# Performance work log

Hardware: AMD Instinct MI355X
Metric: run time of the kernel (lower is better)

## Reference

```python
import jax, jax.numpy as jnp
import numpy as np

C_CURV = 0.1            # curvature k
SC = float(np.sqrt(C_CURV))
EPS = 1e-7


def _mobius_add(x, y, c):
    x2 = jnp.sum(x * x, -1, keepdims=True)
    y2 = jnp.sum(y * y, -1, keepdims=True)
    xy = jnp.sum(x * y, -1, keepdims=True)
    num = (1 + 2 * c * xy + c * y2) * x + (1 - c * x2) * y
    den = 1 + 2 * c * xy + c * c * x2 * y2
    return num / jnp.maximum(den, 1e-12)


def _mobius_scalarmul(r, x, c):
    sc = jnp.sqrt(c)
    n = jnp.linalg.norm(x, axis=-1, keepdims=True)
    t = jnp.clip(sc * n, EPS, 1.0 - 1e-6)
    return jnp.tanh(r * jnp.arctanh(t)) * x / jnp.maximum(sc * n, EPS)


def setup_inputs() -> dict:
    key = jax.random.key(0)
    k0, k1, k2, k3, k4 = jax.random.split(key, 5)
    B, N, V, D, NC = 64, 1024, 50257, 128, 10
    token_ids = jax.random.randint(k0, (B, N), 0, V)
    mask = jax.random.randint(k1, (B, N), 0, 2).astype(bool)
    emb = (jax.random.normal(k2, (V, D), jnp.float32) * 0.02).at[0].set(0.0)  # pad_id=0 row zeroed
    Wo = jax.random.normal(k3, (D, D + 1), jnp.float32) / np.sqrt(D + 1)
    bo = jnp.zeros((D,), jnp.float32)
    Wf = jax.random.normal(k4, (NC, D), jnp.float32) / np.sqrt(D)
    bf = jnp.zeros((NC,), jnp.float32)
    return {"token_ids": token_ids, "mask": mask, "emb": emb, "Wo": Wo, "bo": bo, "Wf": Wf, "bf": bf}


def reference(token_ids, mask, emb, Wo, bo, Wf, bf):
    c, sc = C_CURV, SC
    D = emb.shape[1]
    # embedding lookup (tangent vectors at origin)
    v = emb[token_ids]                                            # (B,N,D)
    # Lorentz expmap0 -> hyperboloid points in D+1
    nv = jnp.maximum(jnp.linalg.norm(v, axis=-1, keepdims=True), EPS)
    x = jnp.concatenate([jnp.cosh(sc * nv) / sc,
                         jnp.sinh(sc * nv) * v / (sc * nv)], -1)  # (B,N,D+1)
    # single-head attention, scores = -<xi,xj>_L (Lorentz inner), masked softmax
    sgn = jnp.concatenate([-jnp.ones((1,)), jnp.ones((D,))]).astype(x.dtype)
    scores = -jnp.einsum('bid,bjd->bij', x * sgn, x) / np.sqrt(D + 1)
    scores = jnp.where(mask[:, None, :], scores, -1e9)
    w = jax.nn.softmax(scores, axis=-1)
    # riemannian value aggregation: Lorentz centroid (weighted sum renormalized to hyperboloid)
    mu = jnp.einsum('bij,bjd->bid', w, x)
    inner = jnp.einsum('bid,d,bid->bi', mu, sgn, mu)
    mu = mu / (sc * jnp.sqrt(jnp.maximum(-inner, EPS))[..., None])
    # output projection (D+1 -> D) then Poincare expmap0 so points lie in the ball
    u = jnp.einsum('bid,od->bio', mu, Wo) + bo                    # (B,N,D)
    nu = jnp.maximum(jnp.linalg.norm(u, axis=-1, keepdims=True), EPS)
    y = jnp.tanh(sc * nu) * u / (sc * nu)                         # (B,N,D) in ball
    # sequential masked Mobius pooling: left-fold mobius_add over valid tokens, then scalarmul 1/n
    def step(acc, xm):
        xi, mi = xm                                               # (B,D), (B,)
        new = _mobius_add(acc, xi, c)
        return jnp.where(mi[:, None], new, acc), None
    acc0 = jnp.zeros_like(y[:, 0, :])
    acc, _ = jax.lax.scan(step, acc0, (jnp.swapaxes(y, 0, 1), jnp.swapaxes(mask, 0, 1)))
    cnt = jnp.sum(mask, axis=1)
    r = (1.0 / jnp.maximum(cnt, 1))[:, None].astype(y.dtype)
    pooled = _mobius_scalarmul(r, acc, c)
    pooled = jnp.where((cnt > 0)[:, None], pooled, y[:, 0, :])    # empty rows fall back to first token
    # LorentzMLR head: logmap0 then linear
    npn = jnp.maximum(jnp.linalg.norm(pooled, axis=-1, keepdims=True), EPS)
    t = jnp.clip(sc * npn, EPS, 1.0 - 1e-6)
    vlog = jnp.arctanh(t) * pooled / (sc * npn)
    return vlog @ Wf.T + bf                                       # (B, num_classes)
```

## Files before the change

### kernel.cpp

```cpp
#include <hip/hip_runtime.h>
#include <math.h>

#define B_    64
#define N_    1024
#define D_    128
#define DP1   129
#define NC_   10
#define QB    128
#define KT    32
#define SCf   0.31622776601683794f
#define SCALE 0.08804509063256238f

typedef __bf16 bf16x8 __attribute__((ext_vector_type(8)));
typedef float  f32x16 __attribute__((ext_vector_type(16)));
typedef unsigned long long ull;

#define MFMA(a, b, c) __builtin_amdgcn_mfma_f32_32x32x16_bf16((a), (b), (c), 0, 0, 0)

static __device__ __forceinline__ float dpp_add_step(float f, int ctrl, int rmask) {
    if (ctrl == 0x111) { int t = __builtin_amdgcn_update_dpp(0, __builtin_bit_cast(int, f), 0x111, 0xf, 0xf, true); return f + __builtin_bit_cast(float, t); }
    if (ctrl == 0x112) { int t = __builtin_amdgcn_update_dpp(0, __builtin_bit_cast(int, f), 0x112, 0xf, 0xf, true); return f + __builtin_bit_cast(float, t); }
    if (ctrl == 0x114) { int t = __builtin_amdgcn_update_dpp(0, __builtin_bit_cast(int, f), 0x114, 0xf, 0xf, true); return f + __builtin_bit_cast(float, t); }
    if (ctrl == 0x118) { int t = __builtin_amdgcn_update_dpp(0, __builtin_bit_cast(int, f), 0x118, 0xf, 0xf, true); return f + __builtin_bit_cast(float, t); }
    if (ctrl == 0x142 && rmask == 0xa) { int t = __builtin_amdgcn_update_dpp(0, __builtin_bit_cast(int, f), 0x142, 0xa, 0xf, true); return f + __builtin_bit_cast(float, t); }
    { int t = __builtin_amdgcn_update_dpp(0, __builtin_bit_cast(int, f), 0x143, 0xc, 0xf, true); return f + __builtin_bit_cast(float, t); }
}

static __device__ __forceinline__ float wave_sum64(float f) {
    f = dpp_add_step(f, 0x111, 0xf);
    f = dpp_add_step(f, 0x112, 0xf);
    f = dpp_add_step(f, 0x114, 0xf);
    f = dpp_add_step(f, 0x118, 0xf);
    f = dpp_add_step(f, 0x142, 0xa);
    f = dpp_add_step(f, 0x143, 0xc);
    return __builtin_bit_cast(float, __builtin_amdgcn_readlane(__builtin_bit_cast(int, f), 63));
}

static __device__ __forceinline__ float half_sum32(float f, int half) {
    f = dpp_add_step(f, 0x111, 0xf);
    f = dpp_add_step(f, 0x112, 0xf);
    f = dpp_add_step(f, 0x114, 0xf);
    f = dpp_add_step(f, 0x118, 0xf);
    f = dpp_add_step(f, 0x142, 0xa);
    float s0 = __builtin_bit_cast(float, __builtin_amdgcn_readlane(__builtin_bit_cast(int, f), 31));
    float s1 = __builtin_bit_cast(float, __builtin_amdgcn_readlane(__builtin_bit_cast(int, f), 63));
    return half ? s1 : s0;
}

static __device__ __forceinline__ float readlane_f(float v, int lane) {
    return __builtin_bit_cast(float, __builtin_amdgcn_readlane(__builtin_bit_cast(int, v), lane));
}

static __device__ __forceinline__ bf16x8 ld_lds8(const __bf16* p) {
    union { bf16x8 v; ull q[2]; } u;
    u.q[0] = *(const ull*)(p);
    u.q[1] = *(const ull*)(p + 4);
    return u.v;
}

__global__ __launch_bounds__(256) void k_detect_mask(const int* __restrict__ mask_w,
                                                     int* __restrict__ flag) {
    __shared__ int bad;
    if (threadIdx.x == 0) bad = 0;
    __syncthreads();
    int local = 0;
    for (int i = threadIdx.x; i < 16384; i += 256) {
        int v = mask_w[i];
        if (v != 0 && v != 1) local = 1;
    }
    if (local) atomicOr(&bad, 1);
    __syncthreads();
    if (threadIdx.x == 0) *flag = bad;
}

static __device__ __forceinline__ int read_mask(const int* mw, int is_i8, int idx) {
    if (is_i8) return (int)((const unsigned char*)mw)[idx];
    return mw[idx];
}

__global__ __launch_bounds__(256) void k_prep_wo(const float* __restrict__ Wo,
                                                 __bf16* __restrict__ Woh,
                                                 __bf16* __restrict__ Wol) {
    int idx = blockIdx.x * 256 + threadIdx.x;
    if (idx >= 128 * 144) return;
    int o = idx / 144, d = idx - o * 144;
    float v = (d < DP1) ? Wo[o * DP1 + d] : 0.f;
    __bf16 h = (__bf16)v;
    Woh[idx] = h;
    Wol[idx] = (__bf16)(v - (float)h);
}

__global__ __launch_bounds__(256) void k_prep(const int* __restrict__ tok,
                                              const float* __restrict__ emb,
                                              __bf16* __restrict__ Xh, __bf16* __restrict__ Xl,
                                              float* __restrict__ X0g, float* __restrict__ X128g) {
    __shared__ float Xf[64][132];
    const int t = threadIdx.x, w = t >> 6, l = t & 63;
    const int base = blockIdx.x * 64;
    for (int it = 0; it < 16; ++it) {
        const int tk = w * 16 + it;
        const int id = tok[base + tk];
        const float2 v = ((const float2*)(emb + (size_t)id * D_))[l];
        float s = wave_sum64(v.x * v.x + v.y * v.y);
        float nv = fmaxf(sqrtf(s), 1e-7f);
        float a = SCf * nv;
        float a2 = a * a;
        float shc, ch;
        if (a < 0.5f) {
            shc = 1.f + a2 * (1.f/6.f) * (1.f + a2 * (1.f/20.f) * (1.f + a2 * (1.f/42.f)));
            ch  = 1.f + a2 * 0.5f * (1.f + a2 * (1.f/12.f) * (1.f + a2 * (1.f/30.f)));
        } else {
            float ea = __expf(a), ei = 1.f / ea;
            ch = 0.5f * (ea + ei);
            shc = 0.5f * (ea - ei) / a;
        }
        Xf[tk][1 + 2 * l] = v.x * shc;
        Xf[tk][2 + 2 * l] = v.y * shc;
        if (l == 0) Xf[tk][0] = ch / SCf;
    }
    __syncthreads();
    const int tk2 = t >> 2, dg = (t & 3) * 32;
    for (int i = 0; i < 32; i += 8) {
        bf16x8 hv, lv;
        #pragma unroll
        for (int j = 0; j < 8; ++j) {
            float f = Xf[tk2][dg + i + j];
            __bf16 h = (__bf16)f;
            hv[j] = h;
            lv[j] = (__bf16)(f - (float)h);
        }
        *(bf16x8*)(Xh + (size_t)(base + tk2) * D_ + dg + i) = hv;
        *(bf16x8*)(Xl + (size_t)(base + tk2) * D_ + dg + i) = lv;
    }
    if (t < 64) {
        X0g[base + t]   = Xf[t][0];
        X128g[base + t] = Xf[t][D_];
    }
}

__global__ __launch_bounds__(256, 2) void k_attn(
        const __bf16* __restrict__ Xh, const __bf16* __restrict__ Xl,
        const float* __restrict__ X0g, const float* __restrict__ X128g,
        const int* __restrict__ mask, const int* __restrict__ mflag,
        const __bf16* __restrict__ Woh, const __bf16* __restrict__ Wol,
        const float* __restrict__ bo,
        float* __restrict__ Y, float* __restrict__ Y2) {
    extern __shared__ char smem[];
    __bf16* KB = (__bf16*)smem;
    __bf16* Pb = (__bf16*)(smem + 33792);
    __shared__ float K0s[2][KT];
    __shared__ float K128s[2][KT];
    __shared__ int   Ms[2][KT];

    const int b    = blockIdx.x;
    const int qb   = blockIdx.y * QB;
    const int t    = threadIdx.x;
    const int w    = t >> 6;
    const int l    = t & 63;
    const int l31  = l & 31;
    const int half = l >> 5;
    const int is8  = *mflag;

    const size_t qrow = (size_t)(b * N_ + qb + w * 32 + l31);
    bf16x8 qfh[8], qfl[8];
    #pragma unroll
    for (int ks = 0; ks < 8; ++ks) {
        qfh[ks] = *(const bf16x8*)(Xh + qrow * D_ + ks * 16 + half * 8);
        qfl[ks] = *(const bf16x8*)(Xl + qrow * D_ + ks * 16 + half * 8);
    }
    float q0[16], q128[16];
    #pragma unroll
    for (int r = 0; r < 16; ++r) {
        const int qr = (r & 3) + 8 * (r >> 2) + 4 * half;
        q0[r]   = X0g[b * N_ + qb + w * 32 + qr];
        q128[r] = X128g[b * N_ + qb + w * 32 + qr];
    }

    const int skey = t >> 3, sck = t & 7;
    bf16x8 svh0, svh1, svl0, svl1;
    float  sK0 = 0.f, sK128 = 0.f;
    int    sM = 0;
    auto ldg_tile = [&](int kt) {
        const size_t kr = (size_t)(b * N_ + kt * KT + skey);
        svh0 = *(const bf16x8*)(Xh + kr * D_ + sck * 16);
        svh1 = *(const bf16x8*)(Xh + kr * D_ + sck * 16 + 8);
        svl0 = *(const bf16x8*)(Xl + kr * D_ + sck * 16);
        svl1 = *(const bf16x8*)(Xl + kr * D_ + sck * 16 + 8);
        if (t < KT) {
            sK0   = X0g[b * N_ + kt * KT + t];
            sK128 = X128g[b * N_ + kt * KT + t];
            sM    = read_mask(mask, is8, b * N_ + kt * KT + t);
        }
    };
    auto st_tile = [&](int buf) {
        __bf16* KH = KB + buf * 8448;
        __bf16* KL = KH + 4224;
        union { bf16x8 v; ull q[2]; } u;
        u.v = svh0; *(ull*)(KH + skey * 132 + sck * 16)      = u.q[0]; *(ull*)(KH + skey * 132 + sck * 16 + 4)  = u.q[1];
        u.v = svh1; *(ull*)(KH + skey * 132 + sck * 16 + 8)  = u.q[0]; *(ull*)(KH + skey * 132 + sck * 16 + 12) = u.q[1];
        u.v = svl0; *(ull*)(KL + skey * 132 + sck * 16)      = u.q[0]; *(ull*)(KL + skey * 132 + sck * 16 + 4)  = u.q[1];
        u.v = svl1; *(ull*)(KL + skey * 132 + sck * 16 + 8)  = u.q[0]; *(ull*)(KL + skey * 132 + sck * 16 + 12) = u.q[1];
        if (t < KT) { K0s[buf][t] = sK0; K128s[buf][t] = sK128; Ms[buf][t] = sM; }
    };

    f32x16 accM[4] = {};
    float  mu128p[16] = {};

    ldg_tile(0);
    st_tile(0);

    for (int kt = 0; kt < N_ / KT; ++kt) {
        __syncthreads();
        const int cur = kt & 1;
        const int ktn = (kt < 31) ? kt + 1 : 31;
        ldg_tile(ktn);

        const __bf16* KH = KB + cur * 8448;
        const __bf16* KL = KH + 4224;

        f32x16 accS = {};
        #pragma unroll
        for (int ks = 0; ks < 8; ++ks) {
            bf16x8 bh = ld_lds8(KH + l31 * 132 + ks * 16 + half * 8);
            bf16x8 bl = ld_lds8(KL + l31 * 132 + ks * 16 + half * 8);
            accS = MFMA(qfh[ks], bh, accS);
            accS = MFMA(qfh[ks], bl, accS);
            accS = MFMA(qfl[ks], bh, accS);
        }
        const float k0v = K0s[cur][l31], k128v = K128s[cur][l31];
        const int   mv  = Ms[cur][l31];
        #pragma unroll
        for (int r = 0; r < 16; ++r) {
            float sc = (2.f * q0[r] * k0v - accS[r] - q128[r] * k128v) * SCALE;
            float e  = mv ? __expf(sc) : 0.f;
            mu128p[r] += e * k128v;
            __bf16 eh = (__bf16)e;
            __bf16 el = (__bf16)(e - (float)eh);
            const int qr = (r & 3) + 8 * (r >> 2) + 4 * half;
            Pb[(w * 2 + 0) * 1152 + qr * 36 + l31] = eh;
            Pb[(w * 2 + 1) * 1152 + qr * 36 + l31] = el;
        }

        #pragma unroll
        for (int ks = 0; ks < 2; ++ks) {
            bf16x8 ah = ld_lds8(Pb + (w * 2 + 0) * 1152 + l31 * 36 + ks * 16 + half * 8);
            bf16x8 al = ld_lds8(Pb + (w * 2 + 1) * 1152 + l31 * 36 + ks * 16 + half * 8);
            #pragma unroll
            for (int nt = 0; nt < 4; ++nt) {
                const int cmp = nt * 32 + l31;
                bf16x8 bh, bl;
                #pragma unroll
                for (int j = 0; j < 8; ++j) {
                    const int key = ks * 16 + half * 8 + j;
                    bh[j] = KH[key * 132 + cmp];
                    bl[j] = KL[key * 132 + cmp];
                }
                accM[nt] = MFMA(ah, bh, accM[nt]);
                accM[nt] = MFMA(ah, bl, accM[nt]);
                accM[nt] = MFMA(al, bh, accM[nt]);
            }
        }

        st_tile(cur ^ 1);
    }

    #pragma unroll
    for (int r = 0; r < 16; ++r) mu128p[r] = half_sum32(mu128p[r], half);
    float rno[16];
    #pragma unroll
    for (int r = 0; r < 16; ++r) {
        float p = 0.f;
        #pragma unroll
        for (int nt = 0; nt < 4; ++nt) p += accM[nt][r] * accM[nt][r];
        if (l31 == 0) p -= 2.f * accM[0][r] * accM[0][r];
        p = half_sum32(p, half);
        float negI = -(p + mu128p[r] * mu128p[r]);
        negI = fmaxf(negI, 1e-7f);
        rno[r] = 1.f / (SCf * sqrtf(negI));
    }
    #pragma unroll
    for (int nt = 0; nt < 4; ++nt)
        #pragma unroll
        for (int r = 0; r < 16; ++r) accM[nt][r] *= rno[r];
    #pragma unroll
    for (int r = 0; r < 16; ++r) mu128p[r] *= rno[r];

    __syncthreads();
    __bf16* MuA = (__bf16*)smem + w * (32 * 148);
    #pragma unroll
    for (int r = 0; r < 16; ++r) {
        const int qr = (r & 3) + 8 * (r >> 2) + 4 * half;
        #pragma unroll
        for (int nt = 0; nt < 4; ++nt)
            MuA[qr * 148 + nt * 32 + l31] = (__bf16)accM[nt][r];
        if (l31 == 0) MuA[qr * 148 + 128] = (__bf16)mu128p[r];
        if (l31 >= 1 && l31 <= 15) MuA[qr * 148 + 128 + l31] = (__bf16)0.f;
    }
    bf16x8 Ah[9];
    #pragma unroll
    for (int ks = 0; ks < 9; ++ks) Ah[ks] = ld_lds8(MuA + l31 * 148 + ks * 16 + half * 8);
    #pragma unroll
    for (int r = 0; r < 16; ++r) {
        const int qr = (r & 3) + 8 * (r >> 2) + 4 * half;
        #pragma unroll
        for (int nt = 0; nt < 4; ++nt) {
            float m = accM[nt][r];
            MuA[qr * 148 + nt * 32 + l31] = (__bf16)(m - (float)(__bf16)m);
        }
        if (l31 == 0) {
            float m = mu128p[r];
            MuA[qr * 148 + 128] = (__bf16)(m - (float)(__bf16)m);
        }
    }
    bf16x8 Al[9];
    #pragma unroll
    for (int ks = 0; ks < 9; ++ks) Al[ks] = ld_lds8(MuA + l31 * 148 + ks * 16 + half * 8);

    f32x16 accU[4] = {};
    #pragma unroll
    for (int ks = 0; ks < 9; ++ks) {
        #pragma unroll
        for (int nt = 0; nt < 4; ++nt) {
            bf16x8 bh = *(const bf16x8*)(Woh + (size_t)(nt * 32 + l31) * 144 + ks * 16 + half * 8);
            bf16x8 bl = *(const bf16x8*)(Wol + (size_t)(nt * 32 + l31) * 144 + ks * 16 + half * 8);
            accU[nt] = MFMA(Ah[ks], bh, accU[nt]);
            accU[nt] = MFMA(Ah[ks], bl, accU[nt]);
            accU[nt] = MFMA(Al[ks], bh, accU[nt]);
        }
    }

    float bov[4];
    #pragma unroll
    for (int nt = 0; nt < 4; ++nt) bov[nt] = bo[nt * 32 + l31];
    #pragma unroll
    for (int r = 0; r < 16; ++r) {
        float p = 0.f;
        #pragma unroll
        for (int nt = 0; nt < 4; ++nt) {
            float uv = accU[nt][r] + bov[nt];
            accU[nt][r] = uv;
            p += uv * uv;
        }
        float nn = half_sum32(p, half);
        float nu = fmaxf(sqrtf(nn), 1e-7f);
        float aa = SCf * nu;
        float cf = tanhf(aa) / aa;
        const int qr = (r & 3) + 8 * (r >> 2) + 4 * half;
        const size_t row = (size_t)(b * N_ + qb + w * 32 + qr);
        #pragma unroll
        for (int nt = 0; nt < 4; ++nt)
            Y[row * D_ + nt * 32 + l31] = accU[nt][r] * cf;
        if (l31 == 0) Y2[row] = nn * cf * cf;
    }
}

__global__ __launch_bounds__(256) void k_gram(const float* __restrict__ Y,
                                              float* __restrict__ G) {
    const int c = blockIdx.x, b = blockIdx.y;
    const int t = threadIdx.x, w = t >> 6, l = t & 63;
    const int l31 = l & 31, half = l >> 5;
    const int rt = w >> 1, ct = w & 1;
    const size_t base = (size_t)(b * N_ + c * 64);
    const float* Ar = Y + (base + rt * 32 + l31) * D_;
    const float* Br = Y + (base + ct * 32 + l31) * D_;
    f32x16 acc = {};
    #pragma unroll
    for (int ks = 0; ks < 8; ++ks) {
        const int c0 = ks * 16 + half * 8;
        float4 a0 = *(const float4*)(Ar + c0);
        float4 a1 = *(const float4*)(Ar + c0 + 4);
        float4 b0 = *(const float4*)(Br + c0);
        float4 b1 = *(const float4*)(Br + c0 + 4);
        float av[8] = {a0.x, a0.y, a0.z, a0.w, a1.x, a1.y, a1.z, a1.w};
        float bv[8] = {b0.x, b0.y, b0.z, b0.w, b1.x, b1.y, b1.z, b1.w};
        bf16x8 ah, al, bh, bl;
        #pragma unroll
        for (int j = 0; j < 8; ++j) {
            __bf16 h = (__bf16)av[j]; ah[j] = h; al[j] = (__bf16)(av[j] - (float)h);
            __bf16 g = (__bf16)bv[j]; bh[j] = g; bl[j] = (__bf16)(bv[j] - (float)g);
        }
        acc = MFMA(ah, bh, acc);
        acc = MFMA(ah, bl, acc);
        acc = MFMA(al, bh, acc);
    }
    float* Gb = G + ((size_t)(b * 16 + c) << 12);
    #pragma unroll
    for (int r = 0; r < 16; ++r) {
        const int row = rt * 32 + (r & 3) + 8 * (r >> 2) + 4 * half;
        Gb[row * 64 + ct * 32 + l31] = acc[r];
    }
}

__global__ __launch_bounds__(64, 1) void k_pool(const float* __restrict__ Y,
                                                const float* __restrict__ Y2,
                                                const float* __restrict__ G,
                                                const int* __restrict__ mask,
                                                const int* __restrict__ mflag,
                                                const float* __restrict__ Wf,
                                                const float* __restrict__ bf_,
                                                float* __restrict__ out) {
    __shared__ float  prt[64][65];
    __shared__ double vb[D_];
    const int b = blockIdx.x, l = threadIdx.x;
    const int is8 = *mflag;

    int cl = 0;
    for (int i = l; i < N_; i += 64) cl += read_mask(mask, is8, b * N_ + i);
    const int cntT = (int)(wave_sum64((float)cl) + 0.5f);

    const float2* __restrict__ Yp = (const float2*)(Y + (size_t)b * N_ * D_) + l;
    const float*  __restrict__ Gp = G + ((size_t)b << 16) + l;
    const float*  __restrict__ Pp = Y2 + b * N_;

    float  GA[64], GB[64];
    float  py2A, py2B;
    int    msA, msB;
    float2 yring[2][16];

    #pragma unroll
    for (int i = 0; i < 64; ++i) GA[i] = Gp[i * 64];
    py2A = Pp[l];
    msA  = read_mask(mask, is8, b * N_ + l);
    #pragma unroll
    for (int k = 0; k < 16; ++k) yring[0][k] = Yp[(size_t)k * 64];

    float U0 = 0.f, U1 = 0.f, g = 0.f, Dh = 1.f, P = 0.f;

    auto chunk = [&](int c, float (&Gc)[64], float (&Gn)[64],
                     float py2c, float& py2n, int msc, int& msn) {
        const int cn = (c < 15) ? c + 1 : 15;
        #pragma unroll
        for (int i = 0; i < 64; ++i) Gn[i] = Gp[cn * 4096 + i * 64];
        py2n = Pp[cn * 64 + l];
        msn  = read_mask(mask, is8, b * N_ + cn * 64 + l);

        #pragma unroll
        for (int q = 0; q < 4; ++q) {
            #pragma unroll
            for (int k = 0; k < 16; ++k) {
                int gs = c * 64 + (q + 1) * 16 + k;
                if (gs > N_ - 1) gs = N_ - 1;
                yring[(q + 1) & 1][k] = Yp[(size_t)gs * 64];
            }
            #pragma unroll
            for (int k = 0; k < 16; ++k) {
                const int ir = q * 16 + k;
                const float2 yv  = yring[q & 1][k];
                const float  Gv  = Gc[ir];
                const float  py2 = readlane_f(py2c, ir);
                const bool   m   = (__builtin_amdgcn_readlane(msc, ir) != 0);
                const float Dsq   = Dh * Dh;
                const float Bh    = fmaf(-0.1f, P, Dsq);
                const float Donep = Dh * fmaf(0.1f, py2, 1.f);
                const float tP    = (0.01f * py2) * P;
                const float puy  = readlane_f(g, ir);
                const float Ahat = fmaf(0.2f, puy, Donep);
                float dh = fmaf(Dh, fmaf(0.2f, puy, Dh), tP);
                dh = fmaxf(dh, 1e-12f * Dsq);
                const float Draw = m ? dh : Dh;
                const float Am   = m ? Ahat : 1.f;
                const float Bm   = m ? Bh   : 0.f;
                const float Pn   = fmaf(Am, fmaf(Am, P, (2.f * Bm) * puy), (Bm * Bm) * py2);
                if ((k & 3) == 3) {
                    const int e = ilogbf(Draw);
                    const float Aef = ldexpf(Am, -e);
                    const float Bef = ldexpf(Bm, -e);
                    Dh = ldexpf(Draw, -e);
                    P  = ldexpf(Pn, -2 * e);
                    g  = fmaf(Aef, g, Bef * Gv);
                    U0 = fmaf(Aef, U0, Bef * yv.x);
                    U1 = fmaf(Aef, U1, Bef * yv.y);
                } else {
                    Dh = Draw;
                    P  = Pn;
                    g  = fmaf(Am, g, Bm * Gv);
                    U0 = fmaf(Am, U0, Bm * yv.x);
                    U1 = fmaf(Am, U1, Bm * yv.y);
                }
            }
        }
        if (c < 15) {
            const int nb = (c + 1) * 64;
            #pragma unroll
            for (int k0 = 0; k0 < 64; k0 += 16) {
                float2 tmp[16];
                #pragma unroll
                for (int k = 0; k < 16; ++k) tmp[k] = Yp[(size_t)(nb + k0 + k) * 64];
                #pragma unroll
                for (int k = 0; k < 16; ++k)
                    prt[k0 + k][l] = fmaf(U0, tmp[k].x, U1 * tmp[k].y);
            }
            float s0 = 0.f, s1 = 0.f, s2 = 0.f, s3 = 0.f;
            #pragma unroll
            for (int p = 0; p < 64; p += 4) {
                s0 += prt[l][p];     s1 += prt[l][p + 1];
                s2 += prt[l][p + 2]; s3 += prt[l][p + 3];
            }
            g = (s0 + s1) + (s2 + s3);
        }
    };

    for (int cc = 0; cc < 8; ++cc) {
        chunk(2 * cc,     GA, GB, py2A, py2B, msA, msB);
        chunk(2 * cc + 1, GB, GA, py2B, py2A, msB, msA);
    }

    const double SCd = 0.31622776601683794;
    const double sD = 1.0 / (double)Dh;
    double a0 = sD * (double)U0, a1 = sD * (double)U1;
    double n2 = fmax((double)P * (sD * sD), 0.0);
    double n = sqrt(n2);
    double tt = SCd * n;
    tt = fmin(fmax(tt, 1e-7), 1.0 - 1e-6);
    int cm = cntT > 0 ? cntT : 1;
    float rf = (float)(1.0 / (double)cm);
    double r = (double)rf;
    double dv = fmax(SCd * n, 1e-7);
    double f = tanh(r * atanh(tt)) / dv;
    double p0 = a0 * f, p1 = a1 * f;
    double q2;
    if (cntT == 0) {
        float2 y0v = *(const float2*)(Y + (size_t)(b * N_) * D_ + 2 * l);
        p0 = y0v.x; p1 = y0v.y;
        q2 = (double)Y2[b * N_];
    } else {
        q2 = f * f * n2;
    }
    double npn = fmax(sqrt(q2), 1e-7);
    double t2 = fmin(fmax(SCd * npn, 1e-7), 1.0 - 1e-6);
    double f2 = atanh(t2) / (SCd * npn);
    vb[2 * l]     = p0 * f2;
    vb[2 * l + 1] = p1 * f2;
    __syncthreads();

    if (l < NC_) {
        double o = (double)bf_[l];
        for (int d = 0; d < D_; ++d) o += vb[d] * (double)Wf[l * D_ + d];
        out[b * NC_ + l] = (float)o;
    }
}

extern "C" void kernel_launch(void* const* d_in, const int* in_sizes, int n_in,
                              void* d_out, int out_size, void* d_ws, size_t ws_size,
                              hipStream_t stream) {
    const int*   tok  = (const int*)d_in[0];
    const int*   mask = (const int*)d_in[1];
    const float* emb  = (const float*)d_in[2];
    const float* Wo   = (const float*)d_in[3];
    const float* bo   = (const float*)d_in[4];
    const float* Wf   = (const float*)d_in[5];
    const float* bf_  = (const float*)d_in[6];
    float* out = (float*)d_out;

    char* wsb = (char*)d_ws;
    __bf16* Xh   = (__bf16*)wsb;
    __bf16* Xl   = (__bf16*)(wsb + 16777216);
    float*  X0g  = (float*)(wsb + 33554432);
    float*  X128g= (float*)(wsb + 33816576);
    __bf16* Woh  = (__bf16*)(wsb + 34078720);
    __bf16* Wol  = (__bf16*)(wsb + 34115584);
    float*  Y    = (float*)(wsb + 34152448);
    float*  Y2   = (float*)(wsb + 67706880);
    int*    flag = (int*)(wsb + 67969024);
    float*  Gram = (float*)wsb;

    k_detect_mask<<<dim3(1), dim3(256), 0, stream>>>(mask, flag);
    k_prep_wo<<<dim3(72), dim3(256), 0, stream>>>(Wo, Woh, Wol);
    k_prep<<<dim3(B_ * N_ / 64), dim3(256), 0, stream>>>(tok, emb, Xh, Xl, X0g, X128g);
    k_attn<<<dim3(B_, N_ / QB), dim3(256), 53760, stream>>>(Xh, Xl, X0g, X128g, mask, flag,
                                                            Woh, Wol, bo, Y, Y2);
    k_gram<<<dim3(16, B_), dim3(256), 0, stream>>>(Y, Gram);
    k_pool<<<dim3(B_), dim3(64), 0, stream>>>(Y, Y2, Gram, mask, flag, Wf, bf_, out);
}
```

Measured before the change: 395.7 us.

## Stage K tiles via direct global-to-LDS loads with XOR-swizzled layout

Stores the split-bf16 hyperboloid embeddings in global memory with a per-row XOR swizzle of 8-element groups, so K tiles can be copied straight into LDS with global_load_lds instead of going through registers and a padded layout. All readers (query fragments, score MFMA operands, transposed value reads) are updated to the swizzled indexing. Dropping the padding shrinks LDS, and launch bounds rise to 3 blocks per SU, with s_setprio raised around MFMA sections. The risk is that the swizzle does not remove bank conflicts on the transposed scalar reads, and that the tighter register budget causes spills.

```diff
diff --git a/kernel.cpp b/kernel.cpp
--- a/kernel.cpp
+++ b/kernel.cpp
@@ -56,6 +56,12 @@
     u.q[0] = *(const ull*)(p);
     u.q[1] = *(const ull*)(p + 4);
     return u.v;
+}
+
+typedef const __attribute__((address_space(1))) unsigned int* glds_gp;
+typedef __attribute__((address_space(3))) unsigned int* glds_lp;
+static __device__ __forceinline__ void glds16(const void* g, void* l) {
+    __builtin_amdgcn_global_load_lds((glds_gp)g, (glds_lp)l, 16, 0, 0);
 }
 
 __global__ __launch_bounds__(256) void k_detect_mask(const int* __restrict__ mask_w,
@@ -120,6 +126,7 @@
     }
     __syncthreads();
     const int tk2 = t >> 2, dg = (t & 3) * 32;
+    const int sw = tk2 & 15;
     for (int i = 0; i < 32; i += 8) {
         bf16x8 hv, lv;
         #pragma unroll
@@ -129,8 +136,10 @@
             hv[j] = h;
             lv[j] = (__bf16)(f - (float)h);
         }
-        *(bf16x8*)(Xh + (size_t)(base + tk2) * D_ + dg + i) = hv;
-        *(bf16x8*)(Xl + (size_t)(base + tk2) * D_ + dg + i) = lv;
+        const int g = (dg + i) >> 3;
+        const int off = ((g ^ sw) << 3);
+        *(bf16x8*)(Xh + (size_t)(base + tk2) * D_ + off) = hv;
+        *(bf16x8*)(Xl + (size_t)(base + tk2) * D_ + off) = lv;
     }
     if (t < 64) {
         X0g[base + t]   = Xf[t][0];
@@ -138,7 +147,7 @@
     }
 }
 
-__global__ __launch_bounds__(256, 2) void k_attn(
+__global__ __launch_bounds__(256, 3) void k_attn(
         const __bf16* __restrict__ Xh, const __bf16* __restrict__ Xl,
         const float* __restrict__ X0g, const float* __restrict__ X128g,
         const int* __restrict__ mask, const int* __restrict__ mflag,
@@ -147,7 +156,7 @@
         float* __restrict__ Y, float* __restrict__ Y2) {
     extern __shared__ char smem[];
     __bf16* KB = (__bf16*)smem;
-    __bf16* Pb = (__bf16*)(smem + 33792);
+    __bf16* Pb = (__bf16*)(smem + 32768);
     __shared__ float K0s[2][KT];
     __shared__ float K128s[2][KT];
     __shared__ int   Ms[2][KT];
@@ -162,11 +171,13 @@
     const int is8  = *mflag;
 
     const size_t qrow = (size_t)(b * N_ + qb + w * 32 + l31);
+    const int swq = l31 & 15;
     bf16x8 qfh[8], qfl[8];
     #pragma unroll
     for (int ks = 0; ks < 8; ++ks) {
-        qfh[ks] = *(const bf16x8*)(Xh + qrow * D_ + ks * 16 + half * 8);
-        qfl[ks] = *(const bf16x8*)(Xl + qrow * D_ + ks * 16 + half * 8);
+        const int off = (((2 * ks + half) ^ swq) << 3);
+        qfh[ks] = *(const bf16x8*)(Xh + qrow * D_ + off);
+        qfl[ks] = *(const bf16x8*)(Xl + qrow * D_ + off);
     }
     float q0[16], q128[16];
     #pragma unroll
@@ -176,57 +187,59 @@
         q128[r] = X128g[b * N_ + qb + w * 32 + qr];
     }
 
-    const int skey = t >> 3, sck = t & 7;
-    bf16x8 svh0, svh1, svl0, svl1;
-    float  sK0 = 0.f, sK128 = 0.f;
-    int    sM = 0;
-    auto ldg_tile = [&](int kt) {
-        const size_t kr = (size_t)(b * N_ + kt * KT + skey);
-        svh0 = *(const bf16x8*)(Xh + kr * D_ + sck * 16);
-        svh1 = *(const bf16x8*)(Xh + kr * D_ + sck * 16 + 8);
-        svl0 = *(const bf16x8*)(Xl + kr * D_ + sck * 16);
-        svl1 = *(const bf16x8*)(Xl + kr * D_ + sck * 16 + 8);
+    auto stage = [&](int kt, int buf) {
+        const size_t gb = (size_t)(b * N_ + kt * KT) * (D_ * 2);
+        const char* gh = (const char*)Xh + gb + w * 2048;
+        const char* gl = (const char*)Xl + gb + w * 2048;
+        char* lh = smem + buf * 16384 + w * 2048;
+        char* ll = smem + buf * 16384 + 8192 + w * 2048;
+        glds16(gh + l * 16,        lh);
+        glds16(gh + 1024 + l * 16, lh + 1024);
+        glds16(gl + l * 16,        ll);
+        glds16(gl + 1024 + l * 16, ll + 1024);
+    };
+    float sK0 = 0.f, sK128 = 0.f;
+    int   sM = 0;
+    auto ldK = [&](int kt) {
         if (t < KT) {
             sK0   = X0g[b * N_ + kt * KT + t];
             sK128 = X128g[b * N_ + kt * KT + t];
             sM    = read_mask(mask, is8, b * N_ + kt * KT + t);
         }
     };
-    auto st_tile = [&](int buf) {
-        __bf16* KH = KB + buf * 8448;
-        __bf16* KL = KH + 4224;
-        union { bf16x8 v; ull q[2]; } u;
-        u.v = svh0; *(ull*)(KH + skey * 132 + sck * 16)      = u.q[0]; *(ull*)(KH + skey * 132 + sck * 16 + 4)  = u.q[1];
-        u.v = svh1; *(ull*)(KH + skey * 132 + sck * 16 + 8)  = u.q[0]; *(ull*)(KH + skey * 132 + sck * 16 + 12) = u.q[1];
-        u.v = svl0; *(ull*)(KL + skey * 132 + sck * 16)      = u.q[0]; *(ull*)(KL + skey * 132 + sck * 16 + 4)  = u.q[1];
-        u.v = svl1; *(ull*)(KL + skey * 132 + sck * 16 + 8)  = u.q[0]; *(ull*)(KL + skey * 132 + sck * 16 + 12) = u.q[1];
+    auto stK = [&](int buf) {
         if (t < KT) { K0s[buf][t] = sK0; K128s[buf][t] = sK128; Ms[buf][t] = sM; }
     };
 
     f32x16 accM[4] = {};
     float  mu128p[16] = {};
 
-    ldg_tile(0);
-    st_tile(0);
+    stage(0, 0);
+    ldK(0);
+    stK(0);
 
     for (int kt = 0; kt < N_ / KT; ++kt) {
         __syncthreads();
         const int cur = kt & 1;
         const int ktn = (kt < 31) ? kt + 1 : 31;
-        ldg_tile(ktn);
-
-        const __bf16* KH = KB + cur * 8448;
-        const __bf16* KL = KH + 4224;
+        stage(ktn, cur ^ 1);
+        ldK(ktn);
+
+        const __bf16* KH = KB + cur * 8192;
+        const __bf16* KL = KH + 4096;
 
         f32x16 accS = {};
+        __builtin_amdgcn_s_setprio(1);
         #pragma unroll
         for (int ks = 0; ks < 8; ++ks) {
-            bf16x8 bh = ld_lds8(KH + l31 * 132 + ks * 16 + half * 8);
-            bf16x8 bl = ld_lds8(KL + l31 * 132 + ks * 16 + half * 8);
+            const int off = (((2 * ks + half) ^ (l31 & 15)) << 3);
+            bf16x8 bh = *(const bf16x8*)(KH + l31 * D_ + off);
+            bf16x8 bl = *(const bf16x8*)(KL + l31 * D_ + off);
             accS = MFMA(qfh[ks], bh, accS);
             accS = MFMA(qfh[ks], bl, accS);
             accS = MFMA(qfl[ks], bh, accS);
         }
+        __builtin_amdgcn_s_setprio(0);
         const float k0v = K0s[cur][l31], k128v = K128s[cur][l31];
         const int   mv  = Ms[cur][l31];
         #pragma unroll
@@ -247,21 +260,25 @@
             bf16x8 al = ld_lds8(Pb + (w * 2 + 1) * 1152 + l31 * 36 + ks * 16 + half * 8);
             #pragma unroll
             for (int nt = 0; nt < 4; ++nt) {
-                const int cmp = nt * 32 + l31;
                 bf16x8 bh, bl;
                 #pragma unroll
                 for (int j = 0; j < 8; ++j) {
                     const int key = ks * 16 + half * 8 + j;
-                    bh[j] = KH[key * 132 + cmp];
-                    bl[j] = KL[key * 132 + cmp];
+                    const int swk = half * 8 + j;
+                    const int idx = key * D_ +
+                        ((((nt * 4 + (l31 >> 3)) ^ swk) << 3) | (l31 & 7));
+                    bh[j] = KH[idx];
+                    bl[j] = KL[idx];
                 }
+                __builtin_amdgcn_s_setprio(1);
                 accM[nt] = MFMA(ah, bh, accM[nt]);
                 accM[nt] = MFMA(ah, bl, accM[nt]);
                 accM[nt] = MFMA(al, bh, accM[nt]);
+                __builtin_amdgcn_s_setprio(0);
             }
         }
 
-        st_tile(cur ^ 1);
+        stK(cur ^ 1);
     }
 
     #pragma unroll
@@ -317,6 +334,7 @@
     for (int ks = 0; ks < 9; ++ks) Al[ks] = ld_lds8(MuA + l31 * 148 + ks * 16 + half * 8);
 
     f32x16 accU[4] = {};
+    __builtin_amdgcn_s_setprio(1);
     #pragma unroll
     for (int ks = 0; ks < 9; ++ks) {
         #pragma unroll
@@ -328,6 +346,7 @@
             accU[nt] = MFMA(Al[ks], bh, accU[nt]);
         }
     }
+    __builtin_amdgcn_s_setprio(0);
 
     float bov[4];
     #pragma unroll
@@ -567,7 +586,7 @@
     k_detect_mask<<<dim3(1), dim3(256), 0, stream>>>(mask, flag);
     k_prep_wo<<<dim3(72), dim3(256), 0, stream>>>(Wo, Woh, Wol);
     k_prep<<<dim3(B_ * N_ / 64), dim3(256), 0, stream>>>(tok, emb, Xh, Xl, X0g, X128g);
-    k_attn<<<dim3(B_, N_ / QB), dim3(256), 53760, stream>>>(Xh, Xl, X0g, X128g, mask, flag,
+    k_attn<<<dim3(B_, N_ / QB), dim3(256), 51200, stream>>>(Xh, Xl, X0g, X128g, mask, flag,
                                                             Woh, Wol, bo, Y, Y2);
     k_gram<<<dim3(16, B_), dim3(256), 0, stream>>>(Y, Gram);
     k_pool<<<dim3(B_), dim3(64), 0, stream>>>(Y, Y2, Gram, mask, flag, Wf, bf_, out);
```

After: 1.069 ms. 170% more time.

## Interleave hi/lo bf16 halves in LDS tiles to halve scalar LDS reads

Applied to the files above, without the earlier changes.

The K tile and probability buffer in LDS now store the high and low bf16 split parts interleaved as 32-bit words instead of in separate arrays. The transposed K reads for the PV product then fetch one dword per key instead of two 16-bit loads, and v_perm repacks the halves into MFMA operands. This is meant to cut the number of LDS instructions in the attention inner loop and reduce shared memory slightly, at the cost of extra permute ALU ops and changed bank-access patterns.

```diff
diff --git a/kernel.cpp b/kernel.cpp
--- a/kernel.cpp
+++ b/kernel.cpp
@@ -13,9 +13,17 @@
 
 typedef __bf16 bf16x8 __attribute__((ext_vector_type(8)));
 typedef float  f32x16 __attribute__((ext_vector_type(16)));
+typedef unsigned int  u32x4v __attribute__((ext_vector_type(4)));
 typedef unsigned long long ull;
 
 #define MFMA(a, b, c) __builtin_amdgcn_mfma_f32_32x32x16_bf16((a), (b), (c), 0, 0, 0)
+
+static __device__ __forceinline__ unsigned pk_lo16(unsigned a, unsigned b) {
+    return __builtin_amdgcn_perm(b, a, 0x05040100u);
+}
+static __device__ __forceinline__ unsigned pk_hi16(unsigned a, unsigned b) {
+    return __builtin_amdgcn_perm(b, a, 0x07060302u);
+}
 
 static __device__ __forceinline__ float dpp_add_step(float f, int ctrl, int rmask) {
     if (ctrl == 0x111) { int t = __builtin_amdgcn_update_dpp(0, __builtin_bit_cast(int, f), 0x111, 0xf, 0xf, true); return f + __builtin_bit_cast(float, t); }
@@ -146,8 +154,8 @@
         const float* __restrict__ bo,
         float* __restrict__ Y, float* __restrict__ Y2) {
     extern __shared__ char smem[];
-    __bf16* KB = (__bf16*)smem;
-    __bf16* Pb = (__bf16*)(smem + 33792);
+    unsigned* KBI = (unsigned*)smem;
+    unsigned* Pbi = (unsigned*)(smem + 33792);
     __shared__ float K0s[2][KT];
     __shared__ float K128s[2][KT];
     __shared__ int   Ms[2][KT];
@@ -193,13 +201,19 @@
         }
     };
     auto st_tile = [&](int buf) {
-        __bf16* KH = KB + buf * 8448;
-        __bf16* KL = KH + 4224;
-        union { bf16x8 v; ull q[2]; } u;
-        u.v = svh0; *(ull*)(KH + skey * 132 + sck * 16)      = u.q[0]; *(ull*)(KH + skey * 132 + sck * 16 + 4)  = u.q[1];
-        u.v = svh1; *(ull*)(KH + skey * 132 + sck * 16 + 8)  = u.q[0]; *(ull*)(KH + skey * 132 + sck * 16 + 12) = u.q[1];
-        u.v = svl0; *(ull*)(KL + skey * 132 + sck * 16)      = u.q[0]; *(ull*)(KL + skey * 132 + sck * 16 + 4)  = u.q[1];
-        u.v = svl1; *(ull*)(KL + skey * 132 + sck * 16 + 8)  = u.q[0]; *(ull*)(KL + skey * 132 + sck * 16 + 12) = u.q[1];
+        unsigned* KI = KBI + buf * 4224;
+        union { bf16x8 v; unsigned d[4]; } H0, H1, L0, L1;
+        H0.v = svh0; H1.v = svh1; L0.v = svl0; L1.v = svl1;
+        u32x4v o0 = { pk_lo16(H0.d[0], L0.d[0]), pk_hi16(H0.d[0], L0.d[0]),
+                      pk_lo16(H0.d[1], L0.d[1]), pk_hi16(H0.d[1], L0.d[1]) };
+        u32x4v o1 = { pk_lo16(H0.d[2], L0.d[2]), pk_hi16(H0.d[2], L0.d[2]),
+                      pk_lo16(H0.d[3], L0.d[3]), pk_hi16(H0.d[3], L0.d[3]) };
+        u32x4v o2 = { pk_lo16(H1.d[0], L1.d[0]), pk_hi16(H1.d[0], L1.d[0]),
+                      pk_lo16(H1.d[1], L1.d[1]), pk_hi16(H1.d[1], L1.d[1]) };
+        u32x4v o3 = { pk_lo16(H1.d[2], L1.d[2]), pk_hi16(H1.d[2], L1.d[2]),
+                      pk_lo16(H1.d[3], L1.d[3]), pk_hi16(H1.d[3], L1.d[3]) };
+        u32x4v* dst = (u32x4v*)(KI + skey * 132 + sck * 16);
+        dst[0] = o0; dst[1] = o1; dst[2] = o2; dst[3] = o3;
         if (t < KT) { K0s[buf][t] = sK0; K128s[buf][t] = sK128; Ms[buf][t] = sM; }
     };
 
@@ -215,17 +229,22 @@
         const int ktn = (kt < 31) ? kt + 1 : 31;
         ldg_tile(ktn);
 
-        const __bf16* KH = KB + cur * 8448;
-        const __bf16* KL = KH + 4224;
+        const unsigned* KI = KBI + cur * 4224;
 
         f32x16 accS = {};
         #pragma unroll
         for (int ks = 0; ks < 8; ++ks) {
-            bf16x8 bh = ld_lds8(KH + l31 * 132 + ks * 16 + half * 8);
-            bf16x8 bl = ld_lds8(KL + l31 * 132 + ks * 16 + half * 8);
-            accS = MFMA(qfh[ks], bh, accS);
-            accS = MFMA(qfh[ks], bl, accS);
-            accS = MFMA(qfl[ks], bh, accS);
+            const unsigned* p = KI + l31 * 132 + ks * 16 + half * 8;
+            u32x4v ua = *(const u32x4v*)(p);
+            u32x4v ub = *(const u32x4v*)(p + 4);
+            union { bf16x8 v; unsigned d[4]; } BH, BL;
+            BH.d[0] = pk_lo16(ua[0], ua[1]); BL.d[0] = pk_hi16(ua[0], ua[1]);
+            BH.d[1] = pk_lo16(ua[2], ua[3]); BL.d[1] = pk_hi16(ua[2], ua[3]);
+            BH.d[2] = pk_lo16(ub[0], ub[1]); BL.d[2] = pk_hi16(ub[0], ub[1]);
+            BH.d[3] = pk_lo16(ub[2], ub[3]); BL.d[3] = pk_hi16(ub[2], ub[3]);
+            accS = MFMA(qfh[ks], BH.v, accS);
+            accS = MFMA(qfh[ks], BL.v, accS);
+            accS = MFMA(qfl[ks], BH.v, accS);
         }
         const float k0v = K0s[cur][l31], k128v = K128s[cur][l31];
         const int   mv  = Ms[cur][l31];
@@ -236,28 +255,36 @@
             mu128p[r] += e * k128v;
             __bf16 eh = (__bf16)e;
             __bf16 el = (__bf16)(e - (float)eh);
+            unsigned pw = (unsigned)__builtin_bit_cast(unsigned short, eh)
+                        | ((unsigned)__builtin_bit_cast(unsigned short, el) << 16);
             const int qr = (r & 3) + 8 * (r >> 2) + 4 * half;
-            Pb[(w * 2 + 0) * 1152 + qr * 36 + l31] = eh;
-            Pb[(w * 2 + 1) * 1152 + qr * 36 + l31] = el;
+            Pbi[w * 1152 + qr * 36 + l31] = pw;
         }
 
         #pragma unroll
         for (int ks = 0; ks < 2; ++ks) {
-            bf16x8 ah = ld_lds8(Pb + (w * 2 + 0) * 1152 + l31 * 36 + ks * 16 + half * 8);
-            bf16x8 al = ld_lds8(Pb + (w * 2 + 1) * 1152 + l31 * 36 + ks * 16 + half * 8);
+            const unsigned* pp = Pbi + w * 1152 + l31 * 36 + ks * 16 + half * 8;
+            u32x4v pa = *(const u32x4v*)(pp);
+            u32x4v pb = *(const u32x4v*)(pp + 4);
+            union { bf16x8 v; unsigned d[4]; } AH, AL;
+            AH.d[0] = pk_lo16(pa[0], pa[1]); AL.d[0] = pk_hi16(pa[0], pa[1]);
+            AH.d[1] = pk_lo16(pa[2], pa[3]); AL.d[1] = pk_hi16(pa[2], pa[3]);
+            AH.d[2] = pk_lo16(pb[0], pb[1]); AL.d[2] = pk_hi16(pb[0], pb[1]);
+            AH.d[3] = pk_lo16(pb[2], pb[3]); AL.d[3] = pk_hi16(pb[2], pb[3]);
             #pragma unroll
             for (int nt = 0; nt < 4; ++nt) {
-                const int cmp = nt * 32 + l31;
-                bf16x8 bh, bl;
+                const unsigned* kb = KI + (ks * 16 + half * 8) * 132 + nt * 32 + l31;
+                unsigned u[8];
                 #pragma unroll
-                for (int j = 0; j < 8; ++j) {
-                    const int key = ks * 16 + half * 8 + j;
-                    bh[j] = KH[key * 132 + cmp];
-                    bl[j] = KL[key * 132 + cmp];
-                }
-                accM[nt] = MFMA(ah, bh, accM[nt]);
-                accM[nt] = MFMA(ah, bl, accM[nt]);
-                accM[nt] = MFMA(al, bh, accM[nt]);
+                for (int j = 0; j < 8; ++j) u[j] = kb[j * 132];
+                union { bf16x8 v; unsigned d[4]; } BH, BL;
+                BH.d[0] = pk_lo16(u[0], u[1]); BL.d[0] = pk_hi16(u[0], u[1]);
+                BH.d[1] = pk_lo16(u[2], u[3]); BL.d[1] = pk_hi16(u[2], u[3]);
+                BH.d[2] = pk_lo16(u[4], u[5]); BL.d[2] = pk_hi16(u[4], u[5]);
+                BH.d[3] = pk_lo16(u[6], u[7]); BL.d[3] = pk_hi16(u[6], u[7]);
+                accM[nt] = MFMA(AH.v, BH.v, accM[nt]);
+                accM[nt] = MFMA(AH.v, BL.v, accM[nt]);
+                accM[nt] = MFMA(AL.v, BH.v, accM[nt]);
             }
         }
 
@@ -567,7 +594,7 @@
     k_detect_mask<<<dim3(1), dim3(256), 0, stream>>>(mask, flag);
     k_prep_wo<<<dim3(72), dim3(256), 0, stream>>>(Wo, Woh, Wol);
     k_prep<<<dim3(B_ * N_ / 64), dim3(256), 0, stream>>>(tok, emb, Xh, Xl, X0g, X128g);
-    k_attn<<<dim3(B_, N_ / QB), dim3(256), 53760, stream>>>(Xh, Xl, X0g, X128g, mask, flag,
+    k_attn<<<dim3(B_, N_ / QB), dim3(256), 52224, stream>>>(Xh, Xl, X0g, X128g, mask, flag,
                                                             Woh, Wol, bo, Y, Y2);
     k_gram<<<dim3(16, B_), dim3(256), 0, stream>>>(Y, Gram);
     k_pool<<<dim3(B_), dim3(64), 0, stream>>>(Y, Y2, Gram, mask, flag, Wf, bf_, out);
```

Result: no change. 392.7 us (-0.8%).
